# Kernel optimization log

Measured on AMD Instinct MI355X. Metric: run time of the kernel, lower is better.

## Reference

```python
import jax, jax.numpy as jnp
import numpy as np

B, NR, M, NL = 1, 384, 4, 128
IN_C, MID_C, OUT_C = 384, 32, 128


def setup_inputs() -> dict:
    key = jax.random.key(0)
    ks = jax.random.split(key, 24)
    s = 0.02
    d = {
        'rec_1d': jax.random.normal(ks[0], (B, NR, IN_C), jnp.float32),
        'lig_1d': jax.random.normal(ks[1], (B, M, NL, IN_C), jnp.float32),
        'pw_rep': jax.random.normal(ks[2], (B, NR + NL, NR + NL, OUT_C), jnp.float32),
        'rl1_w': jax.random.normal(ks[3], (MID_C, IN_C), jnp.float32) * s,
        'rl1_b': jax.random.normal(ks[4], (MID_C,), jnp.float32) * s,
        'rl2_w': jax.random.normal(ks[5], (MID_C, IN_C), jnp.float32) * s,
        'rl2_b': jax.random.normal(ks[6], (MID_C,), jnp.float32) * s,
        'll1_w': jax.random.normal(ks[7], (MID_C, IN_C), jnp.float32) * s,
        'll1_b': jax.random.normal(ks[8], (MID_C,), jnp.float32) * s,
        'll2_w': jax.random.normal(ks[9], (MID_C, IN_C), jnp.float32) * s,
        'll2_b': jax.random.normal(ks[10], (MID_C,), jnp.float32) * s,
        'rr_w': jax.random.normal(ks[11], (OUT_C, MID_C * MID_C), jnp.float32) * s,
        'rr_b': jax.random.normal(ks[12], (OUT_C,), jnp.float32) * s,
        'rl_w': jax.random.normal(ks[13], (OUT_C, MID_C * MID_C), jnp.float32) * s,
        'rl_b': jax.random.normal(ks[14], (OUT_C,), jnp.float32) * s,
        'lr_w': jax.random.normal(ks[15], (OUT_C, MID_C * MID_C), jnp.float32) * s,
        'lr_b': jax.random.normal(ks[16], (OUT_C,), jnp.float32) * s,
        'll_w': jax.random.normal(ks[17], (OUT_C, MID_C * MID_C), jnp.float32) * s,
        'll_b': jax.random.normal(ks[18], (OUT_C,), jnp.float32) * s,
    }
    return d


def reference(rec_1d, lig_1d, pw_rep,
              rl1_w, rl1_b, rl2_w, rl2_b,
              ll1_w, ll1_b, ll2_w, ll2_b,
              rr_w, rr_b, rl_w, rl_b, lr_w, lr_b, ll_w, ll_b):
    mid_c = rl1_w.shape[0]
    m = lig_1d.shape[1]

    # 1D projections (nn.Linear: x @ W.T + b)
    r_i = rec_1d @ rl1_w.T + rl1_b          # [b, NR, mid]
    r_j = rec_1d @ rl2_w.T + rl2_b          # [b, NR, mid]
    l_i = lig_1d @ ll1_w.T + ll1_b          # [b, m, NL, mid]
    l_j = lig_1d @ ll2_w.T + ll2_b          # [b, m, NL, mid]

    # final Linear weights over flattened (x, y) -> [out, x, y] (y fastest, matching .view)
    Wrr = rr_w.reshape(-1, mid_c, mid_c)
    Wrl = rl_w.reshape(-1, mid_c, mid_c)
    Wlr = lr_w.reshape(-1, mid_c, mid_c)
    Wll = ll_w.reshape(-1, mid_c, mid_c)

    # rr[b,i,j,o] = sum_xy r_i[b,i,x] r_j[b,j,y] Wrr[o,x,y]
    # contract projection weight with one factor first (OpenFold trick):
    rr = jnp.einsum('bioy,bjy->bijo', jnp.einsum('bix,oxy->bioy', r_i, Wrr), r_j) + rr_b

    # mean over m commutes with the broadcast outer products for rl/lr
    l_j_mean = l_j.mean(axis=1)             # [b, NL, mid]
    l_i_mean = l_i.mean(axis=1)             # [b, NL, mid]

    rl = jnp.einsum('bioy,bjy->bijo', jnp.einsum('bix,oxy->bioy', r_i, Wrl), l_j_mean) + rl_b

    # lr output is [b, j_lig, i_res, o]: x-axis from r_j, y-axis from l_i
    lr = jnp.einsum('bioy,bjy->bjio', jnp.einsum('bix,oxy->bioy', r_j, Wlr), l_i_mean) + lr_b

    # ll: mean over m of per-copy outer products (not separable)
    ll = jnp.einsum('bmioy,bmjy->bijo', jnp.einsum('bmix,oxy->bmioy', l_i, Wll), l_j) / m + ll_b

    top = jnp.concatenate([rr, rl], axis=2)  # [b, NR, NR+NL, out]
    bot = jnp.concatenate([lr, ll], axis=2)  # [b, NL, NR+NL, out]
    pw_update = jnp.concatenate([top, bot], axis=1).astype(pw_rep.dtype)
    return pw_update
```

## Files before the change

### kernel.cpp

```cpp
#include <hip/hip_runtime.h>

#define NRES 384
#define NLIG 128
#define INC 384
#define OUTC 128
#define NTOT 512

#define WS_RI   0
#define WS_RJ   12288
#define WS_LI   24576
#define WS_LJ   40960
#define WS_BF16 57344

#define BT_RR   0
#define BT_RL   1572864
#define BT_LR   3145728
#define BT_LL   4718592
#define BF_RJ   6815744
#define BF_LJM  6828032
#define BF_LIM  6832128
#define BF_LJ   6836224
#define BF_RI   6852608
#define BF_LI   6864896
#define BW_W    6881280

typedef __bf16 bf16x8 __attribute__((ext_vector_type(8)));
typedef __bf16 bf16x4 __attribute__((ext_vector_type(4)));
typedef float  f32x4  __attribute__((ext_vector_type(4)));

__device__ inline bf16x8 cvt8(const float* p) {
  f32x4 a = *(const f32x4*)p, b = *(const f32x4*)(p + 4);
  bf16x8 r;
  r[0] = (__bf16)a[0]; r[1] = (__bf16)a[1]; r[2] = (__bf16)a[2]; r[3] = (__bf16)a[3];
  r[4] = (__bf16)b[0]; r[5] = (__bf16)b[1]; r[6] = (__bf16)b[2]; r[7] = (__bf16)b[3];
  return r;
}

__global__ __launch_bounds__(256) void kP_proj(
    const float* __restrict__ rec, const float* __restrict__ lig,
    const float* __restrict__ rl1w, const float* __restrict__ rl1b,
    const float* __restrict__ rl2w, const float* __restrict__ rl2b,
    const float* __restrict__ ll1w, const float* __restrict__ ll1b,
    const float* __restrict__ ll2w, const float* __restrict__ ll2b,
    const float* __restrict__ Wrr, const float* __restrict__ Wrl,
    const float* __restrict__ Wlr, const float* __restrict__ Wll,
    float* __restrict__ ws) {
  __shared__ float lds[32 * 33];
  int b = blockIdx.x, t = threadIdx.x;
  __bf16* B16 = (__bf16*)(ws + WS_BF16);
  if (b >= 28) {
    int bb = b - 28;
    int tt = bb >> 7, o = bb & 127;
    const float* W = tt == 0 ? Wrr : tt == 1 ? Wrl : tt == 2 ? Wlr : Wll;
    __bf16* Wb = B16 + BW_W + tt * 131072;
#pragma unroll
    for (int k = 0; k < 4; ++k) {
      int idx = k * 256 + t;
      int x = idx >> 5, y = idx & 31;
      lds[y * 33 + x] = W[(size_t)o * 1024 + idx];
    }
    __syncthreads();
#pragma unroll
    for (int k = 0; k < 4; ++k) {
      int idx = k * 256 + t;
      int y = idx >> 5, x = idx & 31;
      Wb[(size_t)(o * 32 + y) * 32 + x] = (__bf16)lds[y * 33 + x];
    }
    return;
  }
  int l = t & 63, w = t >> 6;
  int lr16 = l & 15, lq = l >> 4;
  int pair = w >> 1, rh = w & 1;

  const float* in;
  const float *w1, *b1, *w2, *b2;
  float *o1, *o2;
  __bf16 *bf1, *bf2;
  int row0;
  if (b < 12) {
    row0 = b * 32;
    in = rec; w1 = rl1w; b1 = rl1b; w2 = rl2w; b2 = rl2b;
    o1 = ws + WS_RI; o2 = ws + WS_RJ;
    bf1 = B16 + BF_RI; bf2 = B16 + BF_RJ;
  } else {
    row0 = (b - 12) * 32;
    in = lig; w1 = ll1w; b1 = ll1b; w2 = ll2w; b2 = ll2b;
    o1 = ws + WS_LI; o2 = ws + WS_LJ;
    bf1 = B16 + BF_LI; bf2 = B16 + BF_LJ;
  }
  const float* wsrc = pair ? w2 : w1;
  const float* bsrc = pair ? b2 : b1;
  float* osrc = pair ? o2 : o1;
  __bf16* bdst = pair ? bf2 : bf1;
  int arow = row0 + rh * 16 + lr16;

  f32x4 acc[2];
#pragma unroll
  for (int ci = 0; ci < 2; ++ci) acc[ci] = (f32x4){0.f, 0.f, 0.f, 0.f};
  for (int ks = 0; ks < 12; ++ks) {
    bf16x8 af = cvt8(in + (size_t)arow * INC + ks * 32 + lq * 8);
#pragma unroll
    for (int ci = 0; ci < 2; ++ci) {
      int ch = ci * 16 + lr16;
      bf16x8 bf = cvt8(wsrc + (size_t)ch * INC + ks * 32 + lq * 8);
      acc[ci] = __builtin_amdgcn_mfma_f32_16x16x32_bf16(af, bf, acc[ci], 0, 0, 0);
    }
  }
#pragma unroll
  for (int ci = 0; ci < 2; ++ci) {
    int c = ci * 16 + lr16;
    float bias = bsrc[c];
#pragma unroll
    for (int e = 0; e < 4; ++e) {
      int r = row0 + rh * 16 + 4 * lq + e;
      float v = acc[ci][e] + bias;
      osrc[r * 32 + c] = v;
      bdst[r * 32 + c] = (__bf16)v;
    }
  }
}

__global__ __launch_bounds__(256) void k2_makeA(float* __restrict__ ws) {
  int b = blockIdx.x, t = threadIdx.x;
  __bf16* B16 = (__bf16*)(ws + WS_BF16);
  if (b >= 256) {
    const float* lj = ws + WS_LJ;
    const float* li = ws + WS_LI;
    __bf16* dm = B16 + BF_LJM;
    __bf16* di = B16 + BF_LIM;
    for (int k = 0; k < 16; ++k) {
      int idx = k * 256 + t;
      dm[idx] = (__bf16)(0.25f * (lj[idx] + lj[4096 + idx] + lj[8192 + idx] + lj[12288 + idx]));
      di[idx] = (__bf16)(0.25f * (li[idx] + li[4096 + idx] + li[8192 + idx] + li[12288 + idx]));
    }
    return;
  }
  int tt = b >> 6, sub = b & 63;
  int nt = sub >> 2, mq = sub & 3;
  const __bf16* facB;
  __bf16* At;
  int M;
  if (tt == 0)      { facB = B16 + BF_RI; At = B16 + BT_RR; M = 384; }
  else if (tt == 1) { facB = B16 + BF_RI; At = B16 + BT_RL; M = 384; }
  else if (tt == 2) { facB = B16 + BF_RJ; At = B16 + BT_LR; M = 384; }
  else              { facB = B16 + BF_LI; At = B16 + BT_LL; M = 512; }
  const __bf16* Wb = B16 + BW_W + tt * 131072;
  int l = t & 63, w = t >> 6;
  int lr16 = l & 15, lq = l >> 4;
  int n0w = nt * 256 + w * 64;
  int mtiles = M >> 6;
  int m0 = mq * (M >> 2);

  bf16x8 wv[4];
#pragma unroll
  for (int q = 0; q < 4; ++q)
    wv[q] = *(const bf16x8*)(Wb + (size_t)(n0w + q * 16 + lr16) * 32 + lq * 8);

  for (int mt = 0; mt < mtiles; ++mt) {
    bf16x8 fv = *(const bf16x8*)(facB + (size_t)(m0 + mt * 16 + lr16) * 32 + lq * 8);
    f32x4 acc[4];
#pragma unroll
    for (int q = 0; q < 4; ++q) acc[q] = (f32x4){0.f, 0.f, 0.f, 0.f};
#pragma unroll
    for (int q = 0; q < 4; ++q)
      acc[q] = __builtin_amdgcn_mfma_f32_16x16x32_bf16(wv[q], fv, acc[q], 0, 0, 0);
    int m = m0 + mt * 16 + lr16;
#pragma unroll
    for (int q = 0; q < 4; ++q) {
      bf16x4 v;
#pragma unroll
      for (int e = 0; e < 4; ++e) v[e] = (__bf16)acc[q][e];
      *(bf16x4*)(At + (size_t)m * 4096 + n0w + q * 16 + 4 * lq) = v;
    }
  }
}

__global__ __launch_bounds__(256) void k3_mfma(
    const float* __restrict__ ws, float* __restrict__ out,
    const float* __restrict__ rrb, const float* __restrict__ rlb,
    const float* __restrict__ lrb, const float* __restrict__ llb) {
  const __bf16* B16 = (const __bf16*)(ws + WS_BF16);
  int b = blockIdx.x, t = threadIdx.x;
  int l = t & 63, w = t >> 6;
  int lr16 = l & 15, lq = l >> 4;

  if (b < 1920) {
    const __bf16* At;
    const __bf16* fc;
    const float* bias;
    float* outp;
    size_t jstr;
    if (b < 1152) {
      int i = b / 3, jt = b - 3 * i;
      At = B16 + BT_RR + (size_t)i * 4096;
      fc = B16 + BF_RJ + jt * 4096;
      bias = rrb; outp = out + ((size_t)i * NTOT + jt * 128) * OUTC; jstr = OUTC;
    } else if (b < 1536) {
      int i = b - 1152;
      At = B16 + BT_RL + (size_t)i * 4096;
      fc = B16 + BF_LJM;
      bias = rlb; outp = out + ((size_t)i * NTOT + NRES) * OUTC; jstr = OUTC;
    } else {
      int i = b - 1536;
      At = B16 + BT_LR + (size_t)i * 4096;
      fc = B16 + BF_LIM;
      bias = lrb; outp = out + (size_t)NRES * NTOT * OUTC + (size_t)i * OUTC;
      jstr = (size_t)NTOT * OUTC;
    }
    bf16x8 fj[2];
#pragma unroll
    for (int jj = 0; jj < 2; ++jj)
      fj[jj] = *(const bf16x8*)(fc + (size_t)(w * 32 + jj * 16 + lr16) * 32 + lq * 8);
    f32x4 acc[2][8];
#pragma unroll
    for (int jj = 0; jj < 2; ++jj)
#pragma unroll
      for (int ot = 0; ot < 8; ++ot) acc[jj][ot] = (f32x4){0.f, 0.f, 0.f, 0.f};
#pragma unroll
    for (int oc = 0; oc < 2; ++oc) {
      bf16x8 av[4];
#pragma unroll
      for (int o4 = 0; o4 < 4; ++o4)
        av[o4] = *(const bf16x8*)(At + (size_t)((oc * 4 + o4) * 16 + lr16) * 32 + lq * 8);
#pragma unroll
      for (int jj = 0; jj < 2; ++jj)
#pragma unroll
        for (int o4 = 0; o4 < 4; ++o4)
          acc[jj][oc * 4 + o4] =
              __builtin_amdgcn_mfma_f32_16x16x32_bf16(av[o4], fj[jj], acc[jj][oc * 4 + o4], 0, 0, 0);
    }
#pragma unroll
    for (int jj = 0; jj < 2; ++jj) {
      int j = w * 32 + jj * 16 + lr16;
#pragma unroll
      for (int ot = 0; ot < 8; ++ot) {
        f32x4 b4 = *(const f32x4*)&bias[ot * 16 + 4 * lq];
        f32x4 v = acc[jj][ot] + b4;
        *(f32x4*)&outp[(size_t)j * jstr + ot * 16 + 4 * lq] = v;
      }
    }
  } else {
    int il = b - 1920;
    f32x4 acc[2][8];
#pragma unroll
    for (int jj = 0; jj < 2; ++jj)
#pragma unroll
      for (int ot = 0; ot < 8; ++ot) acc[jj][ot] = (f32x4){0.f, 0.f, 0.f, 0.f};
    for (int m = 0; m < 4; ++m) {
      const __bf16* At = B16 + BT_LL + (size_t)(m * 128 + il) * 4096;
      const __bf16* fc = B16 + BF_LJ + m * 4096;
      bf16x8 fj[2];
#pragma unroll
      for (int jj = 0; jj < 2; ++jj)
        fj[jj] = *(const bf16x8*)(fc + (size_t)(w * 32 + jj * 16 + lr16) * 32 + lq * 8);
#pragma unroll
      for (int oc = 0; oc < 2; ++oc) {
        bf16x8 av[4];
#pragma unroll
        for (int o4 = 0; o4 < 4; ++o4)
          av[o4] = *(const bf16x8*)(At + (size_t)((oc * 4 + o4) * 16 + lr16) * 32 + lq * 8);
#pragma unroll
        for (int jj = 0; jj < 2; ++jj)
#pragma unroll
          for (int o4 = 0; o4 < 4; ++o4)
            acc[jj][oc * 4 + o4] =
                __builtin_amdgcn_mfma_f32_16x16x32_bf16(av[o4], fj[jj], acc[jj][oc * 4 + o4], 0, 0, 0);
      }
    }
    float* outp = out + ((size_t)(NRES + il) * NTOT + NRES) * OUTC;
#pragma unroll
    for (int jj = 0; jj < 2; ++jj) {
      int j = w * 32 + jj * 16 + lr16;
#pragma unroll
      for (int ot = 0; ot < 8; ++ot) {
        f32x4 b4 = *(const f32x4*)&llb[ot * 16 + 4 * lq];
        f32x4 v = 0.25f * acc[jj][ot] + b4;
        *(f32x4*)&outp[(size_t)j * OUTC + ot * 16 + 4 * lq] = v;
      }
    }
  }
}

extern "C" void kernel_launch(void* const* d_in, const int* in_sizes, int n_in,
                              void* d_out, int out_size, void* d_ws, size_t ws_size,
                              hipStream_t stream) {
  const float* rec  = (const float*)d_in[0];
  const float* lig  = (const float*)d_in[1];
  const float* rl1w = (const float*)d_in[3];
  const float* rl1b = (const float*)d_in[4];
  const float* rl2w = (const float*)d_in[5];
  const float* rl2b = (const float*)d_in[6];
  const float* ll1w = (const float*)d_in[7];
  const float* ll1b = (const float*)d_in[8];
  const float* ll2w = (const float*)d_in[9];
  const float* ll2b = (const float*)d_in[10];
  const float* rrw  = (const float*)d_in[11];
  const float* rrb  = (const float*)d_in[12];
  const float* rlw  = (const float*)d_in[13];
  const float* rlb  = (const float*)d_in[14];
  const float* lrw  = (const float*)d_in[15];
  const float* lrb  = (const float*)d_in[16];
  const float* llw  = (const float*)d_in[17];
  const float* llb  = (const float*)d_in[18];
  float* out = (float*)d_out;
  float* ws  = (float*)d_ws;

  hipLaunchKernelGGL(kP_proj, dim3(540), dim3(256), 0, stream,
                     rec, lig, rl1w, rl1b, rl2w, rl2b, ll1w, ll1b, ll2w, ll2b,
                     rrw, rlw, lrw, llw, ws);
  hipLaunchKernelGGL(k2_makeA, dim3(257), dim3(256), 0, stream, ws);
  hipLaunchKernelGGL(k3_mfma, dim3(2048), dim3(256), 0, stream,
                     ws, out, rrb, rlb, lrb, llb);
}
```

Before: 52.15 us.

## Merge projection and A-build kernels via software grid barrier

Fuses the projection/weight-transpose kernel and the A-matrix construction kernel into one persistent launch of 540 blocks, separated by an atomic-counter grid barrier. A memset clears the counter each call. The aim is to remove one kernel launch and its inter-kernel gap. It relies on all 540 blocks being co-resident, which the launch bounds of 3 blocks per CU are meant to ensure, and otherwise risks deadlock. It also adds the cost of the barrier spin and the memset.

```diff
diff --git a/kernel.cpp b/kernel.cpp
--- a/kernel.cpp
+++ b/kernel.cpp
@@ -5,12 +5,14 @@
 #define INC 384
 #define OUTC 128
 #define NTOT 512
+#define PGRID 540
 
 #define WS_RI   0
 #define WS_RJ   12288
 #define WS_LI   24576
 #define WS_LJ   40960
 #define WS_BF16 57344
+#define WS_CNT  3760128
 
 #define BT_RR   0
 #define BT_RL   1572864
@@ -36,7 +38,21 @@
   return r;
 }
 
-__global__ __launch_bounds__(256) void kP_proj(
+__device__ __forceinline__ void grid_barrier(unsigned* cnt, unsigned target) {
+  __syncthreads();
+  if (threadIdx.x == 0) {
+    __hip_atomic_fetch_add(cnt, 1u, __ATOMIC_ACQ_REL, __HIP_MEMORY_SCOPE_AGENT);
+    unsigned v;
+    do {
+      __builtin_amdgcn_s_sleep(2);
+      v = __hip_atomic_load(cnt, __ATOMIC_RELAXED, __HIP_MEMORY_SCOPE_AGENT);
+    } while (v < target);
+  }
+  __syncthreads();
+  __threadfence();
+}
+
+__global__ __launch_bounds__(256, 3) void kPrep(
     const float* __restrict__ rec, const float* __restrict__ lig,
     const float* __restrict__ rl1w, const float* __restrict__ rl1b,
     const float* __restrict__ rl2w, const float* __restrict__ rl2b,
@@ -46,9 +62,61 @@
     const float* __restrict__ Wlr, const float* __restrict__ Wll,
     float* __restrict__ ws) {
   __shared__ float lds[32 * 33];
+  unsigned* cnt = (unsigned*)(ws + WS_CNT);
   int b = blockIdx.x, t = threadIdx.x;
   __bf16* B16 = (__bf16*)(ws + WS_BF16);
-  if (b >= 28) {
+  int l = t & 63, w = t >> 6;
+  int lr16 = l & 15, lq = l >> 4;
+
+  if (b < 28) {
+    int pair = w >> 1, rh = w & 1;
+    const float* in;
+    const float *w1, *b1, *w2, *b2;
+    float *o1, *o2;
+    __bf16 *bf1, *bf2;
+    int row0;
+    if (b < 12) {
+      row0 = b * 32;
+      in = rec; w1 = rl1w; b1 = rl1b; w2 = rl2w; b2 = rl2b;
+      o1 = ws + WS_RI; o2 = ws + WS_RJ;
+      bf1 = B16 + BF_RI; bf2 = B16 + BF_RJ;
+    } else {
+      row0 = (b - 12) * 32;
+      in = lig; w1 = ll1w; b1 = ll1b; w2 = ll2w; b2 = ll2b;
+      o1 = ws + WS_LI; o2 = ws + WS_LJ;
+      bf1 = B16 + BF_LI; bf2 = B16 + BF_LJ;
+    }
+    const float* wsrc = pair ? w2 : w1;
+    const float* bsrc = pair ? b2 : b1;
+    float* osrc = pair ? o2 : o1;
+    __bf16* bdst = pair ? bf2 : bf1;
+    int arow = row0 + rh * 16 + lr16;
+
+    f32x4 acc[2];
+#pragma unroll
+    for (int ci = 0; ci < 2; ++ci) acc[ci] = (f32x4){0.f, 0.f, 0.f, 0.f};
+    for (int ks = 0; ks < 12; ++ks) {
+      bf16x8 af = cvt8(in + (size_t)arow * INC + ks * 32 + lq * 8);
+#pragma unroll
+      for (int ci = 0; ci < 2; ++ci) {
+        int ch = ci * 16 + lr16;
+        bf16x8 bf = cvt8(wsrc + (size_t)ch * INC + ks * 32 + lq * 8);
+        acc[ci] = __builtin_amdgcn_mfma_f32_16x16x32_bf16(af, bf, acc[ci], 0, 0, 0);
+      }
+    }
+#pragma unroll
+    for (int ci = 0; ci < 2; ++ci) {
+      int c = ci * 16 + lr16;
+      float bias = bsrc[c];
+#pragma unroll
+      for (int e = 0; e < 4; ++e) {
+        int r = row0 + rh * 16 + 4 * lq + e;
+        float v = acc[ci][e] + bias;
+        osrc[r * 32 + c] = v;
+        bdst[r * 32 + c] = (__bf16)v;
+      }
+    }
+  } else {
     int bb = b - 28;
     int tt = bb >> 7, o = bb & 127;
     const float* W = tt == 0 ? Wrr : tt == 1 ? Wrl : tt == 2 ? Wlr : Wll;
@@ -66,64 +134,47 @@
       int y = idx >> 5, x = idx & 31;
       Wb[(size_t)(o * 32 + y) * 32 + x] = (__bf16)lds[y * 33 + x];
     }
-    return;
   }
-  int l = t & 63, w = t >> 6;
-  int lr16 = l & 15, lq = l >> 4;
-  int pair = w >> 1, rh = w & 1;
-
-  const float* in;
-  const float *w1, *b1, *w2, *b2;
-  float *o1, *o2;
-  __bf16 *bf1, *bf2;
-  int row0;
-  if (b < 12) {
-    row0 = b * 32;
-    in = rec; w1 = rl1w; b1 = rl1b; w2 = rl2w; b2 = rl2b;
-    o1 = ws + WS_RI; o2 = ws + WS_RJ;
-    bf1 = B16 + BF_RI; bf2 = B16 + BF_RJ;
-  } else {
-    row0 = (b - 12) * 32;
-    in = lig; w1 = ll1w; b1 = ll1b; w2 = ll2w; b2 = ll2b;
-    o1 = ws + WS_LI; o2 = ws + WS_LJ;
-    bf1 = B16 + BF_LI; bf2 = B16 + BF_LJ;
-  }
-  const float* wsrc = pair ? w2 : w1;
-  const float* bsrc = pair ? b2 : b1;
-  float* osrc = pair ? o2 : o1;
-  __bf16* bdst = pair ? bf2 : bf1;
-  int arow = row0 + rh * 16 + lr16;
-
-  f32x4 acc[2];
-#pragma unroll
-  for (int ci = 0; ci < 2; ++ci) acc[ci] = (f32x4){0.f, 0.f, 0.f, 0.f};
-  for (int ks = 0; ks < 12; ++ks) {
-    bf16x8 af = cvt8(in + (size_t)arow * INC + ks * 32 + lq * 8);
-#pragma unroll
-    for (int ci = 0; ci < 2; ++ci) {
-      int ch = ci * 16 + lr16;
-      bf16x8 bf = cvt8(wsrc + (size_t)ch * INC + ks * 32 + lq * 8);
-      acc[ci] = __builtin_amdgcn_mfma_f32_16x16x32_bf16(af, bf, acc[ci], 0, 0, 0);
-    }
-  }
-#pragma unroll
-  for (int ci = 0; ci < 2; ++ci) {
-    int c = ci * 16 + lr16;
-    float bias = bsrc[c];
-#pragma unroll
-    for (int e = 0; e < 4; ++e) {
-      int r = row0 + rh * 16 + 4 * lq + e;
-      float v = acc[ci][e] + bias;
-      osrc[r * 32 + c] = v;
-      bdst[r * 32 + c] = (__bf16)v;
-    }
-  }
-}
-
-__global__ __launch_bounds__(256) void k2_makeA(float* __restrict__ ws) {
-  int b = blockIdx.x, t = threadIdx.x;
-  __bf16* B16 = (__bf16*)(ws + WS_BF16);
-  if (b >= 256) {
+  grid_barrier(cnt, PGRID);
+
+  if (b < 256) {
+    int tt = b >> 6, sub = b & 63;
+    int nt = sub >> 2, mq = sub & 3;
+    const __bf16* facB;
+    __bf16* At;
+    int M;
+    if (tt == 0)      { facB = B16 + BF_RI; At = B16 + BT_RR; M = 384; }
+    else if (tt == 1) { facB = B16 + BF_RI; At = B16 + BT_RL; M = 384; }
+    else if (tt == 2) { facB = B16 + BF_RJ; At = B16 + BT_LR; M = 384; }
+    else              { facB = B16 + BF_LI; At = B16 + BT_LL; M = 512; }
+    const __bf16* Wb = B16 + BW_W + tt * 131072;
+    int n0w = nt * 256 + w * 64;
+    int mtiles = M >> 6;
+    int m0 = mq * (M >> 2);
+
+    bf16x8 wv[4];
+#pragma unroll
+    for (int q = 0; q < 4; ++q)
+      wv[q] = *(const bf16x8*)(Wb + (size_t)(n0w + q * 16 + lr16) * 32 + lq * 8);
+
+    for (int mt = 0; mt < mtiles; ++mt) {
+      bf16x8 fv = *(const bf16x8*)(facB + (size_t)(m0 + mt * 16 + lr16) * 32 + lq * 8);
+      f32x4 acc[4];
+#pragma unroll
+      for (int q = 0; q < 4; ++q) acc[q] = (f32x4){0.f, 0.f, 0.f, 0.f};
+#pragma unroll
+      for (int q = 0; q < 4; ++q)
+        acc[q] = __builtin_amdgcn_mfma_f32_16x16x32_bf16(wv[q], fv, acc[q], 0, 0, 0);
+      int m = m0 + mt * 16 + lr16;
+#pragma unroll
+      for (int q = 0; q < 4; ++q) {
+        bf16x4 v;
+#pragma unroll
+        for (int e = 0; e < 4; ++e) v[e] = (__bf16)acc[q][e];
+        *(bf16x4*)(At + (size_t)m * 4096 + n0w + q * 16 + 4 * lq) = v;
+      }
+    }
+  } else if (b == 256) {
     const float* lj = ws + WS_LJ;
     const float* li = ws + WS_LI;
     __bf16* dm = B16 + BF_LJM;
@@ -132,45 +183,6 @@
       int idx = k * 256 + t;
       dm[idx] = (__bf16)(0.25f * (lj[idx] + lj[4096 + idx] + lj[8192 + idx] + lj[12288 + idx]));
       di[idx] = (__bf16)(0.25f * (li[idx] + li[4096 + idx] + li[8192 + idx] + li[12288 + idx]));
-    }
-    return;
-  }
-  int tt = b >> 6, sub = b & 63;
-  int nt = sub >> 2, mq = sub & 3;
-  const __bf16* facB;
-  __bf16* At;
-  int M;
-  if (tt == 0)      { facB = B16 + BF_RI; At = B16 + BT_RR; M = 384; }
-  else if (tt == 1) { facB = B16 + BF_RI; At = B16 + BT_RL; M = 384; }
-  else if (tt == 2) { facB = B16 + BF_RJ; At = B16 + BT_LR; M = 384; }
-  else              { facB = B16 + BF_LI; At = B16 + BT_LL; M = 512; }
-  const __bf16* Wb = B16 + BW_W + tt * 131072;
-  int l = t & 63, w = t >> 6;
-  int lr16 = l & 15, lq = l >> 4;
-  int n0w = nt * 256 + w * 64;
-  int mtiles = M >> 6;
-  int m0 = mq * (M >> 2);
-
-  bf16x8 wv[4];
-#pragma unroll
-  for (int q = 0; q < 4; ++q)
-    wv[q] = *(const bf16x8*)(Wb + (size_t)(n0w + q * 16 + lr16) * 32 + lq * 8);
-
-  for (int mt = 0; mt < mtiles; ++mt) {
-    bf16x8 fv = *(const bf16x8*)(facB + (size_t)(m0 + mt * 16 + lr16) * 32 + lq * 8);
-    f32x4 acc[4];
-#pragma unroll
-    for (int q = 0; q < 4; ++q) acc[q] = (f32x4){0.f, 0.f, 0.f, 0.f};
-#pragma unroll
-    for (int q = 0; q < 4; ++q)
-      acc[q] = __builtin_amdgcn_mfma_f32_16x16x32_bf16(wv[q], fv, acc[q], 0, 0, 0);
-    int m = m0 + mt * 16 + lr16;
-#pragma unroll
-    for (int q = 0; q < 4; ++q) {
-      bf16x4 v;
-#pragma unroll
-      for (int e = 0; e < 4; ++e) v[e] = (__bf16)acc[q][e];
-      *(bf16x4*)(At + (size_t)m * 4096 + n0w + q * 16 + 4 * lq) = v;
     }
   }
 }
@@ -305,10 +317,11 @@
   float* out = (float*)d_out;
   float* ws  = (float*)d_ws;
 
-  hipLaunchKernelGGL(kP_proj, dim3(540), dim3(256), 0, stream,
+  hipMemsetAsync((char*)d_ws + (size_t)WS_CNT * 4, 0, 64, stream);
+
+  hipLaunchKernelGGL(kPrep, dim3(PGRID), dim3(256), 0, stream,
                      rec, lig, rl1w, rl1b, rl2w, rl2b, ll1w, ll1b, ll2w, ll2b,
                      rrw, rlw, lrw, llw, ws);
-  hipLaunchKernelGGL(k2_makeA, dim3(257), dim3(256), 0, stream, ws);
   hipLaunchKernelGGL(k3_mfma, dim3(2048), dim3(256), 0, stream,
                      ws, out, rrb, rlb, lrb, llb);
 }
```

Result: slower. 112.7 us (+116.1%).

## Fuse A-tensor construction and mean reductions into the output MFMA kernel

Applied to the files above, without the earlier changes.

Removes the intermediate kernel that materialized large bf16 A tensors in global memory. Each output block now computes its own A tile in shared memory from the projected factor and bf16 weights, and computes the ligand means on the fly. This eliminates a launch and large global write/read traffic, at the cost of redundant per-block scalar compute (rr tiles rebuilt per j-tile) and extra barriers.

```diff
diff --git a/kernel.cpp b/kernel.cpp
--- a/kernel.cpp
+++ b/kernel.cpp
@@ -12,13 +12,7 @@
 #define WS_LJ   40960
 #define WS_BF16 57344
 
-#define BT_RR   0
-#define BT_RL   1572864
-#define BT_LR   3145728
-#define BT_LL   4718592
 #define BF_RJ   6815744
-#define BF_LJM  6828032
-#define BF_LIM  6832128
 #define BF_LJ   6836224
 #define BF_RI   6852608
 #define BF_LI   6864896
@@ -120,58 +114,29 @@
   }
 }
 
-__global__ __launch_bounds__(256) void k2_makeA(float* __restrict__ ws) {
-  int b = blockIdx.x, t = threadIdx.x;
-  __bf16* B16 = (__bf16*)(ws + WS_BF16);
-  if (b >= 256) {
-    const float* lj = ws + WS_LJ;
-    const float* li = ws + WS_LI;
-    __bf16* dm = B16 + BF_LJM;
-    __bf16* di = B16 + BF_LIM;
-    for (int k = 0; k < 16; ++k) {
-      int idx = k * 256 + t;
-      dm[idx] = (__bf16)(0.25f * (lj[idx] + lj[4096 + idx] + lj[8192 + idx] + lj[12288 + idx]));
-      di[idx] = (__bf16)(0.25f * (li[idx] + li[4096 + idx] + li[8192 + idx] + li[12288 + idx]));
-    }
-    return;
-  }
-  int tt = b >> 6, sub = b & 63;
-  int nt = sub >> 2, mq = sub & 3;
-  const __bf16* facB;
-  __bf16* At;
-  int M;
-  if (tt == 0)      { facB = B16 + BF_RI; At = B16 + BT_RR; M = 384; }
-  else if (tt == 1) { facB = B16 + BF_RI; At = B16 + BT_RL; M = 384; }
-  else if (tt == 2) { facB = B16 + BF_RJ; At = B16 + BT_LR; M = 384; }
-  else              { facB = B16 + BF_LI; At = B16 + BT_LL; M = 512; }
-  const __bf16* Wb = B16 + BW_W + tt * 131072;
+__device__ __forceinline__ void build_at(__bf16* AT, const float* fac,
+                                         const __bf16* Wb, int t) {
+  float f[32];
+#pragma unroll
+  for (int i = 0; i < 8; ++i) {
+    f32x4 v = *(const f32x4*)(fac + i * 4);
+    f[i * 4 + 0] = v[0]; f[i * 4 + 1] = v[1];
+    f[i * 4 + 2] = v[2]; f[i * 4 + 3] = v[3];
+  }
   int l = t & 63, w = t >> 6;
-  int lr16 = l & 15, lq = l >> 4;
-  int n0w = nt * 256 + w * 64;
-  int mtiles = M >> 6;
-  int m0 = mq * (M >> 2);
-
-  bf16x8 wv[4];
-#pragma unroll
-  for (int q = 0; q < 4; ++q)
-    wv[q] = *(const bf16x8*)(Wb + (size_t)(n0w + q * 16 + lr16) * 32 + lq * 8);
-
-  for (int mt = 0; mt < mtiles; ++mt) {
-    bf16x8 fv = *(const bf16x8*)(facB + (size_t)(m0 + mt * 16 + lr16) * 32 + lq * 8);
-    f32x4 acc[4];
-#pragma unroll
-    for (int q = 0; q < 4; ++q) acc[q] = (f32x4){0.f, 0.f, 0.f, 0.f};
-#pragma unroll
-    for (int q = 0; q < 4; ++q)
-      acc[q] = __builtin_amdgcn_mfma_f32_16x16x32_bf16(wv[q], fv, acc[q], 0, 0, 0);
-    int m = m0 + mt * 16 + lr16;
-#pragma unroll
-    for (int q = 0; q < 4; ++q) {
-      bf16x4 v;
-#pragma unroll
-      for (int e = 0; e < 4; ++e) v[e] = (__bf16)acc[q][e];
-      *(bf16x4*)(At + (size_t)m * 4096 + n0w + q * 16 + 4 * lq) = v;
-    }
+  int base = w * 1024;
+#pragma unroll 4
+  for (int k = 0; k < 16; ++k) {
+    int n = base + k * 64 + l;
+    const __bf16* wr = Wb + (size_t)n * 32;
+    float acc = 0.f;
+#pragma unroll
+    for (int xc = 0; xc < 4; ++xc) {
+      bf16x8 wv = *(const bf16x8*)(wr + xc * 8);
+#pragma unroll
+      for (int e = 0; e < 8; ++e) acc += f[xc * 8 + e] * (float)wv[e];
+    }
+    AT[n] = (__bf16)acc;
   }
 }
 
@@ -179,38 +144,65 @@
     const float* __restrict__ ws, float* __restrict__ out,
     const float* __restrict__ rrb, const float* __restrict__ rlb,
     const float* __restrict__ lrb, const float* __restrict__ llb) {
+  __shared__ __bf16 AT[4096];
   const __bf16* B16 = (const __bf16*)(ws + WS_BF16);
   int b = blockIdx.x, t = threadIdx.x;
   int l = t & 63, w = t >> 6;
   int lr16 = l & 15, lq = l >> 4;
 
   if (b < 1920) {
-    const __bf16* At;
-    const __bf16* fc;
     const float* bias;
     float* outp;
     size_t jstr;
+    bf16x8 fj[2];
     if (b < 1152) {
       int i = b / 3, jt = b - 3 * i;
-      At = B16 + BT_RR + (size_t)i * 4096;
-      fc = B16 + BF_RJ + jt * 4096;
+      build_at(AT, ws + WS_RI + i * 32, B16 + BW_W + 0 * 131072, t);
+      const __bf16* fc = B16 + BF_RJ + jt * 4096;
+#pragma unroll
+      for (int jj = 0; jj < 2; ++jj)
+        fj[jj] = *(const bf16x8*)(fc + (size_t)(w * 32 + jj * 16 + lr16) * 32 + lq * 8);
       bias = rrb; outp = out + ((size_t)i * NTOT + jt * 128) * OUTC; jstr = OUTC;
     } else if (b < 1536) {
       int i = b - 1152;
-      At = B16 + BT_RL + (size_t)i * 4096;
-      fc = B16 + BF_LJM;
+      build_at(AT, ws + WS_RI + i * 32, B16 + BW_W + 1 * 131072, t);
+      const __bf16* lj = B16 + BF_LJ;
+#pragma unroll
+      for (int jj = 0; jj < 2; ++jj) {
+        size_t off = (size_t)(w * 32 + jj * 16 + lr16) * 32 + lq * 8;
+        float s[8] = {0, 0, 0, 0, 0, 0, 0, 0};
+#pragma unroll
+        for (int mm = 0; mm < 4; ++mm) {
+          bf16x8 v = *(const bf16x8*)(lj + mm * 4096 + off);
+#pragma unroll
+          for (int e = 0; e < 8; ++e) s[e] += (float)v[e];
+        }
+#pragma unroll
+        for (int e = 0; e < 8; ++e) fj[jj][e] = (__bf16)(0.25f * s[e]);
+      }
       bias = rlb; outp = out + ((size_t)i * NTOT + NRES) * OUTC; jstr = OUTC;
     } else {
       int i = b - 1536;
-      At = B16 + BT_LR + (size_t)i * 4096;
-      fc = B16 + BF_LIM;
+      build_at(AT, ws + WS_RJ + i * 32, B16 + BW_W + 2 * 131072, t);
+      const __bf16* li = B16 + BF_LI;
+#pragma unroll
+      for (int jj = 0; jj < 2; ++jj) {
+        size_t off = (size_t)(w * 32 + jj * 16 + lr16) * 32 + lq * 8;
+        float s[8] = {0, 0, 0, 0, 0, 0, 0, 0};
+#pragma unroll
+        for (int mm = 0; mm < 4; ++mm) {
+          bf16x8 v = *(const bf16x8*)(li + mm * 4096 + off);
+#pragma unroll
+          for (int e = 0; e < 8; ++e) s[e] += (float)v[e];
+        }
+#pragma unroll
+        for (int e = 0; e < 8; ++e) fj[jj][e] = (__bf16)(0.25f * s[e]);
+      }
       bias = lrb; outp = out + (size_t)NRES * NTOT * OUTC + (size_t)i * OUTC;
       jstr = (size_t)NTOT * OUTC;
     }
-    bf16x8 fj[2];
-#pragma unroll
-    for (int jj = 0; jj < 2; ++jj)
-      fj[jj] = *(const bf16x8*)(fc + (size_t)(w * 32 + jj * 16 + lr16) * 32 + lq * 8);
+    __syncthreads();
+
     f32x4 acc[2][8];
 #pragma unroll
     for (int jj = 0; jj < 2; ++jj)
@@ -221,7 +213,7 @@
       bf16x8 av[4];
 #pragma unroll
       for (int o4 = 0; o4 < 4; ++o4)
-        av[o4] = *(const bf16x8*)(At + (size_t)((oc * 4 + o4) * 16 + lr16) * 32 + lq * 8);
+        av[o4] = *(const bf16x8*)(AT + (size_t)((oc * 4 + o4) * 16 + lr16) * 32 + lq * 8);
 #pragma unroll
       for (int jj = 0; jj < 2; ++jj)
 #pragma unroll
@@ -241,13 +233,15 @@
     }
   } else {
     int il = b - 1920;
+    const __bf16* Wb = B16 + BW_W + 3 * 131072;
     f32x4 acc[2][8];
 #pragma unroll
     for (int jj = 0; jj < 2; ++jj)
 #pragma unroll
       for (int ot = 0; ot < 8; ++ot) acc[jj][ot] = (f32x4){0.f, 0.f, 0.f, 0.f};
     for (int m = 0; m < 4; ++m) {
-      const __bf16* At = B16 + BT_LL + (size_t)(m * 128 + il) * 4096;
+      build_at(AT, ws + WS_LI + (m * 128 + il) * 32, Wb, t);
+      __syncthreads();
       const __bf16* fc = B16 + BF_LJ + m * 4096;
       bf16x8 fj[2];
 #pragma unroll
@@ -258,7 +252,7 @@
         bf16x8 av[4];
 #pragma unroll
         for (int o4 = 0; o4 < 4; ++o4)
-          av[o4] = *(const bf16x8*)(At + (size_t)((oc * 4 + o4) * 16 + lr16) * 32 + lq * 8);
+          av[o4] = *(const bf16x8*)(AT + (size_t)((oc * 4 + o4) * 16 + lr16) * 32 + lq * 8);
 #pragma unroll
         for (int jj = 0; jj < 2; ++jj)
 #pragma unroll
@@ -266,6 +260,7 @@
             acc[jj][oc * 4 + o4] =
                 __builtin_amdgcn_mfma_f32_16x16x32_bf16(av[o4], fj[jj], acc[jj][oc * 4 + o4], 0, 0, 0);
       }
+      __syncthreads();
     }
     float* outp = out + ((size_t)(NRES + il) * NTOT + NRES) * OUTC;
 #pragma unroll
@@ -308,7 +303,6 @@
   hipLaunchKernelGGL(kP_proj, dim3(540), dim3(256), 0, stream,
                      rec, lig, rl1w, rl1b, rl2w, rl2b, ll1w, ll1b, ll2w, ll2b,
                      rrw, rlw, lrw, llw, ws);
-  hipLaunchKernelGGL(k2_makeA, dim3(257), dim3(256), 0, stream, ws);
   hipLaunchKernelGGL(k3_mfma, dim3(2048), dim3(256), 0, stream,
                      ws, out, rrb, rlb, lrb, llb);
 }
```

Measured after the change: 87.99 us. 68.7% more time.

## Split makeA into one block per 16x256 tile and stage stores through LDS

Applied to the files above, without the earlier changes.

k2_makeA now launches one block per 16-row by 256-column output tile (1664 blocks plus the mean block) instead of 256 blocks that each looped over many row tiles. Each block writes its MFMA results into a padded shared-memory tile, then writes rows out with 16-byte stores, so global writes are wide and contiguous instead of scattered 8-byte stores. This is meant to raise occupancy and store efficiency in the kernel that materializes the intermediate matrices. In exchange, the weight fragments are reloaded once per block and every block pays an extra barrier.

```diff
diff --git a/kernel.cpp b/kernel.cpp
--- a/kernel.cpp
+++ b/kernel.cpp
@@ -120,10 +120,12 @@
   }
 }
 
+#define TSTR2 264
 __global__ __launch_bounds__(256) void k2_makeA(float* __restrict__ ws) {
+  __shared__ __bf16 tile[16 * TSTR2];
   int b = blockIdx.x, t = threadIdx.x;
   __bf16* B16 = (__bf16*)(ws + WS_BF16);
-  if (b >= 256) {
+  if (b >= 1664) {
     const float* lj = ws + WS_LJ;
     const float* li = ws + WS_LI;
     __bf16* dm = B16 + BF_LJM;
@@ -135,43 +137,45 @@
     }
     return;
   }
-  int tt = b >> 6, sub = b & 63;
-  int nt = sub >> 2, mq = sub & 3;
+  int tt, local;
+  if (b < 1152) { tt = b / 384; local = b % 384; }
+  else          { tt = 3;       local = b - 1152; }
+  int nt = local & 15, mt = local >> 4;
   const __bf16* facB;
   __bf16* At;
-  int M;
-  if (tt == 0)      { facB = B16 + BF_RI; At = B16 + BT_RR; M = 384; }
-  else if (tt == 1) { facB = B16 + BF_RI; At = B16 + BT_RL; M = 384; }
-  else if (tt == 2) { facB = B16 + BF_RJ; At = B16 + BT_LR; M = 384; }
-  else              { facB = B16 + BF_LI; At = B16 + BT_LL; M = 512; }
+  if (tt == 0)      { facB = B16 + BF_RI; At = B16 + BT_RR; }
+  else if (tt == 1) { facB = B16 + BF_RI; At = B16 + BT_RL; }
+  else if (tt == 2) { facB = B16 + BF_RJ; At = B16 + BT_LR; }
+  else              { facB = B16 + BF_LI; At = B16 + BT_LL; }
   const __bf16* Wb = B16 + BW_W + tt * 131072;
   int l = t & 63, w = t >> 6;
   int lr16 = l & 15, lq = l >> 4;
-  int n0w = nt * 256 + w * 64;
-  int mtiles = M >> 6;
-  int m0 = mq * (M >> 2);
+  int nw = w * 64, n0 = nt * 256, m0 = mt * 16;
 
   bf16x8 wv[4];
 #pragma unroll
   for (int q = 0; q < 4; ++q)
-    wv[q] = *(const bf16x8*)(Wb + (size_t)(n0w + q * 16 + lr16) * 32 + lq * 8);
-
-  for (int mt = 0; mt < mtiles; ++mt) {
-    bf16x8 fv = *(const bf16x8*)(facB + (size_t)(m0 + mt * 16 + lr16) * 32 + lq * 8);
-    f32x4 acc[4];
-#pragma unroll
-    for (int q = 0; q < 4; ++q) acc[q] = (f32x4){0.f, 0.f, 0.f, 0.f};
-#pragma unroll
-    for (int q = 0; q < 4; ++q)
-      acc[q] = __builtin_amdgcn_mfma_f32_16x16x32_bf16(wv[q], fv, acc[q], 0, 0, 0);
-    int m = m0 + mt * 16 + lr16;
-#pragma unroll
-    for (int q = 0; q < 4; ++q) {
-      bf16x4 v;
-#pragma unroll
-      for (int e = 0; e < 4; ++e) v[e] = (__bf16)acc[q][e];
-      *(bf16x4*)(At + (size_t)m * 4096 + n0w + q * 16 + 4 * lq) = v;
-    }
+    wv[q] = *(const bf16x8*)(Wb + (size_t)(n0 + nw + q * 16 + lr16) * 32 + lq * 8);
+  bf16x8 fv = *(const bf16x8*)(facB + (size_t)(m0 + lr16) * 32 + lq * 8);
+
+  f32x4 acc[4];
+#pragma unroll
+  for (int q = 0; q < 4; ++q) acc[q] = (f32x4){0.f, 0.f, 0.f, 0.f};
+#pragma unroll
+  for (int q = 0; q < 4; ++q)
+    acc[q] = __builtin_amdgcn_mfma_f32_16x16x32_bf16(wv[q], fv, acc[q], 0, 0, 0);
+#pragma unroll
+  for (int q = 0; q < 4; ++q) {
+    bf16x4 v;
+#pragma unroll
+    for (int e = 0; e < 4; ++e) v[e] = (__bf16)acc[q][e];
+    *(bf16x4*)&tile[lr16 * TSTR2 + nw + q * 16 + 4 * lq] = v;
+  }
+  __syncthreads();
+  for (int idx = t; idx < 512; idx += 256) {
+    int m = idx >> 5, nl = (idx & 31) * 8;
+    bf16x8 v = *(const bf16x8*)&tile[m * TSTR2 + nl];
+    *(bf16x8*)(At + (size_t)(m0 + m) * 4096 + n0 + nl) = v;
   }
 }
 
@@ -308,7 +312,7 @@
   hipLaunchKernelGGL(kP_proj, dim3(540), dim3(256), 0, stream,
                      rec, lig, rl1w, rl1b, rl2w, rl2b, ll1w, ll1b, ll2w, ll2b,
                      rrw, rlw, lrw, llw, ws);
-  hipLaunchKernelGGL(k2_makeA, dim3(257), dim3(256), 0, stream, ws);
+  hipLaunchKernelGGL(k2_makeA, dim3(1665), dim3(256), 0, stream, ws);
   hipLaunchKernelGGL(k3_mfma, dim3(2048), dim3(256), 0, stream,
                      ws, out, rrb, rlb, lrb, llb);
 }
```

New measurement: 50.98 us. 1.02x faster.
